# Kernel optimization log

Hardware: AMD Instinct MI355X
Metric: run time of the kernel (lower is better)

The kernel has to match this reference:

```python
import jax, jax.numpy as jnp
import numpy as np

D = 1024
H = 16
HD = D // H
SCALE = HD ** -0.5


def setup_inputs() -> dict:
    key = jax.random.key(0)
    ks = jax.random.split(key, 5)
    x = jax.random.normal(ks[0], (2, 2048, D), dtype=jnp.float32)
    s = 1.0 / np.sqrt(D)
    W_qkv = jax.random.uniform(ks[1], (D, 3 * D), jnp.float32, -s, s)
    b_qkv = jax.random.uniform(ks[2], (3 * D,), jnp.float32, -s, s)
    W_out = jax.random.uniform(ks[3], (D, D), jnp.float32, -s, s)
    b_out = jax.random.uniform(ks[4], (D,), jnp.float32, -s, s)
    return {"x": x, "W_qkv": W_qkv, "b_qkv": b_qkv, "W_out": W_out, "b_out": b_out}


def reference(x, W_qkv, b_qkv, W_out, b_out):
    B, S, _ = x.shape
    qkv = x @ W_qkv + b_qkv                       # [B,S,3D]
    qkv = qkv.reshape(B, S, 3, H, HD)
    q, k, v = jnp.moveaxis(qkv, 2, 0)             # each [B,S,H,HD]
    # scores: [B,H,S,S]
    scores = jnp.einsum("bshd,bthd->bhst", q, k) * SCALE
    attn = jax.nn.softmax(scores, axis=-1)        # dropout is identity in eval mode
    out = jnp.einsum("bhst,bthd->bshd", attn, v)  # [B,S,H,HD]
    out = out.reshape(B, S, H * HD)
    return out @ W_out + b_out
```

## Files before the change

### kernel.cpp

```cpp
#include <hip/hip_runtime.h>

typedef unsigned short u16;
typedef unsigned int   u32;

using short8 = __attribute__((ext_vector_type(8))) short;
using f32x4  = __attribute__((ext_vector_type(4))) float;
using half4  = __attribute__((ext_vector_type(4))) _Float16;
using half8  = __attribute__((ext_vector_type(8))) _Float16;

#define QSCALE 0.18033688011112042f

__device__ __forceinline__ u16 f2bf(float f) {
  u32 u = __float_as_uint(f);
  return (u16)((u + 0x8000u) >> 16);
}
__device__ __forceinline__ u16 f2h(float f) {
  _Float16 h = (_Float16)f;
  return __builtin_bit_cast(u16, h);
}

__device__ __forceinline__ void gld16(const u16* g, u16* l) {
  __builtin_amdgcn_global_load_lds(
      (const __attribute__((address_space(1))) unsigned int*)g,
      (__attribute__((address_space(3))) unsigned int*)l, 16, 0, 0);
}

__global__ __launch_bounds__(256) void cvt_x(const float* __restrict__ in,
                                             u16* __restrict__ out) {
  int idx = blockIdx.x * 256 + threadIdx.x;
  float4 v = reinterpret_cast<const float4*>(in)[idx];
  ushort4 o;
  o.x = f2bf(v.x); o.y = f2bf(v.y); o.z = f2bf(v.z); o.w = f2bf(v.w);
  reinterpret_cast<ushort4*>(out)[idx] = o;
}

__global__ __launch_bounds__(256) void transpose_w(const float* __restrict__ in,
                                                   u16* __restrict__ out,
                                                   int R, int C) {
  __shared__ u32 s[32][33];
  int c0 = blockIdx.x * 32, r0 = blockIdx.y * 32;
  int j = threadIdx.x & 31, i0 = threadIdx.x >> 5;
#pragma unroll
  for (int p = 0; p < 4; ++p) {
    int i = i0 + p * 8;
    s[i][j] = f2bf(in[(size_t)(r0 + i) * C + c0 + j]);
  }
  __syncthreads();
#pragma unroll
  for (int p = 0; p < 4; ++p) {
    int jj = i0 + p * 8;
    out[(size_t)(c0 + jj) * R + r0 + j] = (u16)s[j][jj];
  }
}

template <int EPI, int MT>
__global__ __launch_bounds__(256, 3) void gemm_bt(
    const u16* __restrict__ A, const u16* __restrict__ Bt,
    const float* __restrict__ bias, float* __restrict__ c_out,
    u16* __restrict__ q_out, u16* __restrict__ k_out, u16* __restrict__ vt_out,
    int M, int N, int K) {
  __shared__ __align__(16) u16 As[32 * MT * 32];
  __shared__ __align__(16) u16 Bs[128 * 32];
  const int tid = threadIdx.x;
  const int lane = tid & 63;
  const int wv = tid >> 6;
  const int l16 = lane & 15, quad = lane >> 4;
  const int wm = wv & 1, wn = wv >> 1;
  const int bx = blockIdx.x, by = blockIdx.y;

  const u16* Ab = A + (size_t)by * (32 * MT) * K;
  const u16* Bb = Bt + (size_t)bx * 128 * K;

  const f32x4 fzero = {0.0f, 0.0f, 0.0f, 0.0f};
  f32x4 acc[MT][4];
#pragma unroll
  for (int i = 0; i < MT; ++i)
#pragma unroll
    for (int j = 0; j < 4; ++j) acc[i][j] = fzero;

  for (int k0 = 0; k0 < K; k0 += 32) {
    __syncthreads();
#pragma unroll
    for (int p = 0; p < MT / 2; ++p) {
      int id = p * 256 + tid;
      int row = id >> 2, blk = id & 3;
      int gc = k0 + ((blk ^ (row & 3)) << 3);
      gld16(Ab + (size_t)row * K + gc, &As[id << 3]);
    }
#pragma unroll
    for (int p = 0; p < 2; ++p) {
      int id = p * 256 + tid;
      int row = id >> 2, blk = id & 3;
      int gc = k0 + ((blk ^ (row & 3)) << 3);
      gld16(Bb + (size_t)row * K + gc, &Bs[id << 3]);
    }
    __syncthreads();
    short8 af[MT], bfr[4];
#pragma unroll
    for (int mi = 0; mi < MT; ++mi) {
      int row = wm * (MT * 16) + mi * 16 + l16;
      af[mi] = *reinterpret_cast<const short8*>(&As[row * 32 + ((quad ^ (row & 3)) << 3)]);
    }
#pragma unroll
    for (int ni = 0; ni < 4; ++ni) {
      int row = wn * 64 + ni * 16 + l16;
      bfr[ni] = *reinterpret_cast<const short8*>(&Bs[row * 32 + ((quad ^ (row & 3)) << 3)]);
    }
#pragma unroll
    for (int mi = 0; mi < MT; ++mi)
#pragma unroll
      for (int ni = 0; ni < 4; ++ni)
        acc[mi][ni] = __builtin_amdgcn_mfma_f32_16x16x32_bf16(af[mi], bfr[ni], acc[mi][ni], 0, 0, 0);
  }

#pragma unroll
  for (int mi = 0; mi < MT; ++mi)
#pragma unroll
    for (int ni = 0; ni < 4; ++ni) {
      int col = bx * 128 + wn * 64 + ni * 16 + l16;
      float bv = bias[col];
      int row0 = by * (32 * MT) + wm * (MT * 16) + mi * 16 + quad * 4;
      if (EPI == 1) {
#pragma unroll
        for (int r = 0; r < 4; ++r)
          c_out[(size_t)(row0 + r) * N + col] = acc[mi][ni][r] + bv;
      } else {
        int which = col >> 10, rem = col & 1023;
        int h = rem >> 6, d = rem & 63;
        int b = row0 >> 11, sq0 = row0 & 2047;
        int bh = (b << 4) + h;
        if (which == 2) {
          ushort4 pk;
          pk.x = f2h(acc[mi][ni][0] + bv);
          pk.y = f2h(acc[mi][ni][1] + bv);
          pk.z = f2h(acc[mi][ni][2] + bv);
          pk.w = f2h(acc[mi][ni][3] + bv);
          size_t off = (size_t)bh * 131072 +
                       (((sq0 >> 2) * 16 + (d & 15)) * 16 + ((d >> 4) << 2));
          *reinterpret_cast<ushort4*>(&vt_out[off]) = pk;
        } else {
          size_t base = (size_t)(bh * 2048 + sq0) * 64 + d;
#pragma unroll
          for (int r = 0; r < 4; ++r) {
            float val = acc[mi][ni][r] + bv;
            if (which == 0) q_out[base + r * 64] = f2bf(val * QSCALE);
            else            k_out[base + r * 64] = f2bf(val);
          }
        }
      }
    }
}

__global__ __launch_bounds__(256, 4) void attn(
    const u16* __restrict__ q_buf, const u16* __restrict__ k_buf,
    const u16* __restrict__ vt_buf, u16* __restrict__ o_buf) {
  __shared__ __align__(16) u16 Ks[2][4096];
  __shared__ __align__(16) u16 Vs[2][4096];

  const int tid = threadIdx.x;
  const int lane = tid & 63, w = tid >> 6;
  const int l16 = lane & 15, quad = lane >> 4;
  const int bh = blockIdx.x, q0 = blockIdx.y * 64;

  const u16* qg = q_buf + (size_t)bh * 131072 + (q0 + w * 16) * 64;
  const u16* kg = k_buf + (size_t)bh * 131072;
  const u16* vg = vt_buf + (size_t)bh * 131072;

  short8 qb[2];
#pragma unroll
  for (int kk = 0; kk < 2; ++kk)
    qb[kk] = *reinterpret_cast<const short8*>(qg + l16 * 64 + kk * 32 + quad * 8);

  const int idA = tid, idB = 256 + tid;
  const u16* ksA = kg + (idA >> 3) * 64 + (((idA & 7) ^ ((idA >> 3) & 7)) << 3);
  const u16* ksB = kg + (idB >> 3) * 64 + (((idB & 7) ^ ((idB >> 3) & 7)) << 3);
  const u16* vsA = vg + ((idA ^ ((idA >> 4) & 1)) << 3);
  const u16* vsB = vg + ((idB ^ ((idB >> 4) & 1)) << 3);
  const int ldA = idA << 3, ldB = idB << 3;

  int k0o[4], k1o[4], v0o[4], v1o[4];
#pragma unroll
  for (int t = 0; t < 4; ++t) {
    int rr = t * 16 + l16;
    k0o[t] = rr * 64 + ((quad ^ (rr & 7)) << 3);
    k1o[t] = rr * 64 + (((4 + quad) ^ (rr & 7)) << 3);
    int gb = (t * 4 + quad) * 32 + l16 * 2;
    int sw = (l16 >> 3) & 1;
    v0o[t] = (gb + sw) << 3;
    v1o[t] = (gb + (sw ^ 1)) << 3;
  }

  const f32x4 fzero = {0.0f, 0.0f, 0.0f, 0.0f};
  f32x4 o_acc[4];
  float l_acc = 0.f;
#pragma unroll
  for (int nd = 0; nd < 4; ++nd) o_acc[nd] = fzero;

#define STAGE(BUF)                           \
  do {                                       \
    gld16(ksA, &Ks[BUF][ldA]);               \
    gld16(ksB, &Ks[BUF][ldB]);               \
    gld16(vsA, &Vs[BUF][ldA]);               \
    gld16(vsB, &Vs[BUF][ldB]);               \
    ksA += 4096; ksB += 4096;                \
    vsA += 4096; vsB += 4096;                \
  } while (0)

#define TILE(BUF)                                                         \
  do {                                                                    \
    _Pragma("unroll")                                                     \
    for (int t = 0; t < 4; ++t) {                                         \
      short8 k0f = *reinterpret_cast<const short8*>(&Ks[BUF][k0o[t]]);    \
      short8 k1f = *reinterpret_cast<const short8*>(&Ks[BUF][k1o[t]]);    \
      half8 v0 = *reinterpret_cast<const half8*>(&Vs[BUF][v0o[t]]);       \
      half8 v1 = *reinterpret_cast<const half8*>(&Vs[BUF][v1o[t]]);       \
      half4 vb0 = __builtin_shufflevector(v0, v0, 0, 1, 2, 3);            \
      half4 vb1 = __builtin_shufflevector(v0, v0, 4, 5, 6, 7);            \
      half4 vb2 = __builtin_shufflevector(v1, v1, 0, 1, 2, 3);            \
      half4 vb3 = __builtin_shufflevector(v1, v1, 4, 5, 6, 7);            \
      __builtin_amdgcn_s_setprio(1);                                      \
      f32x4 s = __builtin_amdgcn_mfma_f32_16x16x32_bf16(k0f, qb[0], fzero, 0, 0, 0); \
      s = __builtin_amdgcn_mfma_f32_16x16x32_bf16(k1f, qb[1], s, 0, 0, 0);\
      __builtin_amdgcn_s_setprio(0);                                      \
      float p0 = __builtin_amdgcn_exp2f(s[0]);                            \
      float p1 = __builtin_amdgcn_exp2f(s[1]);                            \
      float p2 = __builtin_amdgcn_exp2f(s[2]);                            \
      float p3 = __builtin_amdgcn_exp2f(s[3]);                            \
      l_acc += (p0 + p1) + (p2 + p3);                                     \
      half4 pa;                                                           \
      pa[0] = (_Float16)p0; pa[1] = (_Float16)p1;                         \
      pa[2] = (_Float16)p2; pa[3] = (_Float16)p3;                         \
      __builtin_amdgcn_s_setprio(1);                                      \
      o_acc[0] = __builtin_amdgcn_mfma_f32_16x16x16f16(pa, vb0, o_acc[0], 0, 0, 0); \
      o_acc[1] = __builtin_amdgcn_mfma_f32_16x16x16f16(pa, vb1, o_acc[1], 0, 0, 0); \
      o_acc[2] = __builtin_amdgcn_mfma_f32_16x16x16f16(pa, vb2, o_acc[2], 0, 0, 0); \
      o_acc[3] = __builtin_amdgcn_mfma_f32_16x16x16f16(pa, vb3, o_acc[3], 0, 0, 0); \
      __builtin_amdgcn_s_setprio(0);                                      \
    }                                                                     \
  } while (0)

  STAGE(0);
  __syncthreads();

  for (int i = 0; i < 32; i += 2) {
    if (i + 1 < 32) STAGE(1);
    TILE(0);
    __syncthreads();
    if (i + 2 < 32) STAGE(0);
    TILE(1);
    __syncthreads();
  }
#undef STAGE
#undef TILE

  l_acc += __shfl_xor(l_acc, 16, 64);
  l_acc += __shfl_xor(l_acc, 32, 64);

  const int b = bh >> 4, h = bh & 15;
  float lv[4];
#pragma unroll
  for (int r = 0; r < 4; ++r)
    lv[r] = __shfl(l_acc, quad * 4 + r, 64);
#pragma unroll
  for (int nd = 0; nd < 4; ++nd) {
#pragma unroll
    for (int r = 0; r < 4; ++r) {
      int sq = q0 + w * 16 + quad * 4 + r;
      o_buf[(size_t)(b * 2048 + sq) * 1024 + h * 64 + nd * 16 + l16] =
          f2bf(o_acc[nd][r] / lv[r]);
    }
  }
}

extern "C" void kernel_launch(void* const* d_in, const int* in_sizes, int n_in,
                              void* d_out, int out_size, void* d_ws, size_t ws_size,
                              hipStream_t stream) {
  (void)in_sizes; (void)n_in; (void)out_size; (void)ws_size;
  const float* x     = (const float*)d_in[0];
  const float* W_qkv = (const float*)d_in[1];
  const float* b_qkv = (const float*)d_in[2];
  const float* W_out = (const float*)d_in[3];
  const float* b_out = (const float*)d_in[4];
  float* out = (float*)d_out;

  char* ws = (char*)d_ws;
  u16* x_bf   = (u16*)(ws);
  u16* wqkv_t = (u16*)(ws + 8388608);
  u16* wout_t = (u16*)(ws + 14680064);
  u16* q_buf  = (u16*)(ws + 16777216);
  u16* k_buf  = (u16*)(ws + 25165824);
  u16* vt_buf = (u16*)(ws + 33554432);
  u16* o_bf   = (u16*)(ws + 41943040);

  cvt_x<<<4096, 256, 0, stream>>>(x, x_bf);
  transpose_w<<<dim3(96, 32), 256, 0, stream>>>(W_qkv, wqkv_t, 1024, 3072);
  transpose_w<<<dim3(32, 32), 256, 0, stream>>>(W_out, wout_t, 1024, 1024);
  gemm_bt<0, 4><<<dim3(24, 32), 256, 0, stream>>>(x_bf, wqkv_t, b_qkv, nullptr,
                                                  q_buf, k_buf, vt_buf, 4096, 3072, 1024);
  attn<<<dim3(32, 32), 256, 0, stream>>>(q_buf, k_buf, vt_buf, o_bf);
  gemm_bt<1, 2><<<dim3(8, 64), 256, 0, stream>>>(o_bf, wout_t, b_out, out,
                                                 nullptr, nullptr, nullptr, 4096, 1024, 1024);
}
```

Before: 189.0 us.

## Add dedicated QKV GEMM with 128x192 tiles and 4-stage LDS pipeline

Replaces the generic gemm_bt call for the QKV projection with a specialized kernel using 128x192 block tiles, a four-deep shared-memory ring buffer fed by direct global-to-LDS loads, and staged vmcnt waits. Loads for future tiles are interleaved between MFMA batches, with s_setprio raising priority around the matrix instructions, so memory latency overlaps compute. The larger tile raises register and LDS use, and occupancy drops to 2 blocks per SM. The grid shrinks to 512 blocks, which may load the 256 CUs unevenly.

```diff
diff --git a/kernel.cpp b/kernel.cpp
--- a/kernel.cpp
+++ b/kernel.cpp
@@ -51,6 +51,151 @@
     int jj = i0 + p * 8;
     out[(size_t)(c0 + jj) * R + r0 + j] = (u16)s[j][jj];
   }
+}
+
+__global__ __launch_bounds__(256, 2) void gemm_qkv(
+    const u16* __restrict__ A, const u16* __restrict__ Bt,
+    const float* __restrict__ bias,
+    u16* __restrict__ q_out, u16* __restrict__ k_out, u16* __restrict__ vt_out) {
+  const int K = 1024;
+  __shared__ __align__(16) u16 As[4][128 * 32];
+  __shared__ __align__(16) u16 Bs[4][192 * 32];
+  const int tid = threadIdx.x;
+  const int lane = tid & 63, wv = tid >> 6;
+  const int l16 = lane & 15, quad = lane >> 4;
+  const int wm = wv & 1, wn = wv >> 1;
+  const int bx = blockIdx.x, by = blockIdx.y;
+
+  const u16* Ab = A + (size_t)by * 128 * K;
+  const u16* Bb = Bt + (size_t)bx * 192 * K;
+
+  const int iA0 = tid, iA1 = 256 + tid;
+  const int iB0 = tid, iB1 = 256 + tid, iB2 = 512 + tid;
+  const u16* sA0 = Ab + (size_t)(iA0 >> 2) * K + (((iA0 & 3) ^ ((iA0 >> 2) & 3)) << 3);
+  const u16* sA1 = Ab + (size_t)(iA1 >> 2) * K + (((iA1 & 3) ^ ((iA1 >> 2) & 3)) << 3);
+  const u16* sB0 = Bb + (size_t)(iB0 >> 2) * K + (((iB0 & 3) ^ ((iB0 >> 2) & 3)) << 3);
+  const u16* sB1 = Bb + (size_t)(iB1 >> 2) * K + (((iB1 & 3) ^ ((iB1 >> 2) & 3)) << 3);
+  const u16* sB2 = Bb + (size_t)(iB2 >> 2) * K + (((iB2 & 3) ^ ((iB2 >> 2) & 3)) << 3);
+  const int dA0 = iA0 << 3, dA1 = iA1 << 3;
+  const int dB0 = iB0 << 3, dB1 = iB1 << 3, dB2 = iB2 << 3;
+
+  int aoff[4], boff[6];
+#pragma unroll
+  for (int mi = 0; mi < 4; ++mi) {
+    int r = wm * 64 + mi * 16 + l16;
+    aoff[mi] = r * 32 + ((quad ^ (r & 3)) << 3);
+  }
+#pragma unroll
+  for (int ni = 0; ni < 6; ++ni) {
+    int r = wn * 96 + ni * 16 + l16;
+    boff[ni] = r * 32 + ((quad ^ (r & 3)) << 3);
+  }
+
+  const f32x4 fzero = {0.0f, 0.0f, 0.0f, 0.0f};
+  f32x4 acc[4][6];
+#pragma unroll
+  for (int i = 0; i < 4; ++i)
+#pragma unroll
+    for (int j = 0; j < 6; ++j) acc[i][j] = fzero;
+
+#define STAGE_A(T)                        \
+  do {                                    \
+    gld16(sA0, &As[T][dA0]);              \
+    gld16(sA1, &As[T][dA1]);              \
+    sA0 += 32; sA1 += 32;                 \
+  } while (0)
+#define STAGE_B(T)                        \
+  do {                                    \
+    gld16(sB0, &Bs[T][dB0]);              \
+    gld16(sB1, &Bs[T][dB1]);              \
+    gld16(sB2, &Bs[T][dB2]);              \
+    sB0 += 32; sB1 += 32; sB2 += 32;      \
+  } while (0)
+#define VM5 asm volatile("s_waitcnt vmcnt(5)" ::: "memory")
+#define VM0 asm volatile("s_waitcnt vmcnt(0)" ::: "memory")
+
+#define GTILE(S, T, DOST, VW)                                              \
+  do {                                                                     \
+    short8 bb[6];                                                          \
+    _Pragma("unroll")                                                      \
+    for (int j = 0; j < 6; ++j)                                            \
+      bb[j] = *reinterpret_cast<const short8*>(&Bs[S][boff[j]]);           \
+    short8 a0 = *reinterpret_cast<const short8*>(&As[S][aoff[0]]);         \
+    short8 a1 = *reinterpret_cast<const short8*>(&As[S][aoff[1]]);         \
+    if (DOST) { STAGE_A(T); }                                              \
+    __builtin_amdgcn_s_barrier();                                          \
+    __builtin_amdgcn_s_setprio(1);                                         \
+    _Pragma("unroll")                                                      \
+    for (int j = 0; j < 6; ++j) {                                          \
+      acc[0][j] = __builtin_amdgcn_mfma_f32_16x16x32_bf16(a0, bb[j], acc[0][j], 0, 0, 0); \
+      acc[1][j] = __builtin_amdgcn_mfma_f32_16x16x32_bf16(a1, bb[j], acc[1][j], 0, 0, 0); \
+    }                                                                      \
+    __builtin_amdgcn_s_setprio(0);                                         \
+    __builtin_amdgcn_s_barrier();                                          \
+    short8 a2 = *reinterpret_cast<const short8*>(&As[S][aoff[2]]);         \
+    short8 a3 = *reinterpret_cast<const short8*>(&As[S][aoff[3]]);         \
+    if (DOST) { STAGE_B(T); }                                              \
+    __builtin_amdgcn_s_barrier();                                          \
+    __builtin_amdgcn_s_setprio(1);                                         \
+    _Pragma("unroll")                                                      \
+    for (int j = 0; j < 6; ++j) {                                          \
+      acc[2][j] = __builtin_amdgcn_mfma_f32_16x16x32_bf16(a2, bb[j], acc[2][j], 0, 0, 0); \
+      acc[3][j] = __builtin_amdgcn_mfma_f32_16x16x32_bf16(a3, bb[j], acc[3][j], 0, 0, 0); \
+    }                                                                      \
+    __builtin_amdgcn_s_setprio(0);                                         \
+    VW;                                                                    \
+    __builtin_amdgcn_s_barrier();                                          \
+  } while (0)
+
+  STAGE_A(0); STAGE_B(0);
+  STAGE_A(1); STAGE_B(1);
+  VM5;
+  __builtin_amdgcn_s_barrier();
+
+  for (int kb = 0; kb < 28; kb += 4) {
+    GTILE(0, 2, 1, VM5);
+    GTILE(1, 3, 1, VM5);
+    GTILE(2, 0, 1, VM5);
+    GTILE(3, 1, 1, VM5);
+  }
+  GTILE(0, 2, 1, VM5);
+  GTILE(1, 3, 1, VM5);
+  GTILE(2, 0, 0, VM0);
+  GTILE(3, 1, 0, ((void)0));
+#undef GTILE
+#undef STAGE_A
+#undef STAGE_B
+
+#pragma unroll
+  for (int mi = 0; mi < 4; ++mi)
+#pragma unroll
+    for (int ni = 0; ni < 6; ++ni) {
+      int col = bx * 192 + wn * 96 + ni * 16 + l16;
+      float bv = bias[col];
+      int row0 = by * 128 + wm * 64 + mi * 16 + quad * 4;
+      int which = col >> 10, rem = col & 1023;
+      int h = rem >> 6, d = rem & 63;
+      int b = row0 >> 11, sq0 = row0 & 2047;
+      int bh = (b << 4) + h;
+      if (which == 2) {
+        ushort4 pk;
+        pk.x = f2h(acc[mi][ni][0] + bv);
+        pk.y = f2h(acc[mi][ni][1] + bv);
+        pk.z = f2h(acc[mi][ni][2] + bv);
+        pk.w = f2h(acc[mi][ni][3] + bv);
+        size_t off = (size_t)bh * 131072 +
+                     (((sq0 >> 2) * 16 + (d & 15)) * 16 + ((d >> 4) << 2));
+        *reinterpret_cast<ushort4*>(&vt_out[off]) = pk;
+      } else {
+        size_t base = (size_t)(bh * 2048 + sq0) * 64 + d;
+#pragma unroll
+        for (int r = 0; r < 4; ++r) {
+          float val = acc[mi][ni][r] + bv;
+          if (which == 0) q_out[base + r * 64] = f2bf(val * QSCALE);
+          else            k_out[base + r * 64] = f2bf(val);
+        }
+      }
+    }
 }
 
 template <int EPI, int MT>
@@ -295,8 +440,8 @@
   cvt_x<<<4096, 256, 0, stream>>>(x, x_bf);
   transpose_w<<<dim3(96, 32), 256, 0, stream>>>(W_qkv, wqkv_t, 1024, 3072);
   transpose_w<<<dim3(32, 32), 256, 0, stream>>>(W_out, wout_t, 1024, 1024);
-  gemm_bt<0, 4><<<dim3(24, 32), 256, 0, stream>>>(x_bf, wqkv_t, b_qkv, nullptr,
-                                                  q_buf, k_buf, vt_buf, 4096, 3072, 1024);
+  gemm_qkv<<<dim3(16, 32), 256, 0, stream>>>(x_bf, wqkv_t, b_qkv,
+                                             q_buf, k_buf, vt_buf);
   attn<<<dim3(32, 32), 256, 0, stream>>>(q_buf, k_buf, vt_buf, o_bf);
   gemm_bt<1, 2><<<dim3(8, 64), 256, 0, stream>>>(o_bf, wout_t, b_out, out,
                                                  nullptr, nullptr, nullptr, 4096, 1024, 1024);
```

New measurement: 188.3 us. Within noise of the previous version (-0.3%).

## Double-buffer GEMM LDS tiles and retile to 64-row blocks with setprio

Applied to the files above, without the earlier changes.

Replaces the single-buffered GEMM with a double-buffered version that issues the next K-slice's global-to-LDS loads before computing the current one, so the loads overlap the MFMA work. Tiles change to 64 rows by NI*32 columns (192 columns for the QKV projection, 64 for the output projection), launch bounds rise to 4 blocks per SM, source pointers are precomputed, and s_setprio wraps the MFMA bursts. The aim is to hide global-load latency and keep more blocks resident. In exchange it doubles LDS per block, and the grids and per-wave register use change.

```diff
diff --git a/kernel.cpp b/kernel.cpp
--- a/kernel.cpp
+++ b/kernel.cpp
@@ -53,73 +53,105 @@
   }
 }
 
-template <int EPI, int MT>
-__global__ __launch_bounds__(256, 3) void gemm_bt(
+template <int EPI, int NI>
+__global__ __launch_bounds__(256, 4) void gemm4(
     const u16* __restrict__ A, const u16* __restrict__ Bt,
     const float* __restrict__ bias, float* __restrict__ c_out,
     u16* __restrict__ q_out, u16* __restrict__ k_out, u16* __restrict__ vt_out,
-    int M, int N, int K) {
-  __shared__ __align__(16) u16 As[32 * MT * 32];
-  __shared__ __align__(16) u16 Bs[128 * 32];
+    int N, int K) {
+  constexpr int BN = NI * 32;
+  constexpr int PB = BN / 64;
+  __shared__ __align__(16) u16 As[2][64 * 32];
+  __shared__ __align__(16) u16 Bs[2][BN * 32];
   const int tid = threadIdx.x;
-  const int lane = tid & 63;
-  const int wv = tid >> 6;
+  const int lane = tid & 63, wv = tid >> 6;
   const int l16 = lane & 15, quad = lane >> 4;
   const int wm = wv & 1, wn = wv >> 1;
   const int bx = blockIdx.x, by = blockIdx.y;
 
-  const u16* Ab = A + (size_t)by * (32 * MT) * K;
-  const u16* Bb = Bt + (size_t)bx * 128 * K;
+  const u16* Ab = A + (size_t)by * 64 * K;
+  const u16* Bb = Bt + (size_t)bx * BN * K;
+
+  const u16* sA = Ab + (size_t)(tid >> 2) * K + (((tid & 3) ^ ((tid >> 2) & 3)) << 3);
+  const int dA = tid << 3;
+  const u16* sB[PB];
+  int dB[PB];
+#pragma unroll
+  for (int p = 0; p < PB; ++p) {
+    int id = p * 256 + tid;
+    sB[p] = Bb + (size_t)(id >> 2) * K + (((id & 3) ^ ((id >> 2) & 3)) << 3);
+    dB[p] = id << 3;
+  }
+
+  int aoff[2], boff[NI];
+#pragma unroll
+  for (int mi = 0; mi < 2; ++mi) {
+    int r = wm * 32 + mi * 16 + l16;
+    aoff[mi] = r * 32 + ((quad ^ (r & 3)) << 3);
+  }
+#pragma unroll
+  for (int ni = 0; ni < NI; ++ni) {
+    int r = wn * (BN / 2) + ni * 16 + l16;
+    boff[ni] = r * 32 + ((quad ^ (r & 3)) << 3);
+  }
 
   const f32x4 fzero = {0.0f, 0.0f, 0.0f, 0.0f};
-  f32x4 acc[MT][4];
-#pragma unroll
-  for (int i = 0; i < MT; ++i)
-#pragma unroll
-    for (int j = 0; j < 4; ++j) acc[i][j] = fzero;
-
-  for (int k0 = 0; k0 < K; k0 += 32) {
+  f32x4 acc[2][NI];
+#pragma unroll
+  for (int i = 0; i < 2; ++i)
+#pragma unroll
+    for (int j = 0; j < NI; ++j) acc[i][j] = fzero;
+
+#define STAGE4(T)                                            \
+  do {                                                       \
+    gld16(sA, &As[T][dA]);                                   \
+    sA += 32;                                                \
+    _Pragma("unroll")                                        \
+    for (int p = 0; p < PB; ++p) {                           \
+      gld16(sB[p], &Bs[T][dB[p]]);                           \
+      sB[p] += 32;                                           \
+    }                                                        \
+  } while (0)
+
+#define KSTEP4(S)                                                          \
+  do {                                                                     \
+    short8 a0 = *reinterpret_cast<const short8*>(&As[S][aoff[0]]);         \
+    short8 a1 = *reinterpret_cast<const short8*>(&As[S][aoff[1]]);         \
+    short8 bb[NI];                                                         \
+    _Pragma("unroll")                                                      \
+    for (int j = 0; j < NI; ++j)                                           \
+      bb[j] = *reinterpret_cast<const short8*>(&Bs[S][boff[j]]);           \
+    __builtin_amdgcn_s_setprio(1);                                         \
+    _Pragma("unroll")                                                      \
+    for (int j = 0; j < NI; ++j) {                                         \
+      acc[0][j] = __builtin_amdgcn_mfma_f32_16x16x32_bf16(a0, bb[j], acc[0][j], 0, 0, 0); \
+      acc[1][j] = __builtin_amdgcn_mfma_f32_16x16x32_bf16(a1, bb[j], acc[1][j], 0, 0, 0); \
+    }                                                                      \
+    __builtin_amdgcn_s_setprio(0);                                         \
+  } while (0)
+
+  STAGE4(0);
+  __syncthreads();
+
+  const int NK = K / 32;
+  for (int ks = 0; ks < NK; ks += 2) {
+    if (ks + 1 < NK) STAGE4(1);
+    KSTEP4(0);
     __syncthreads();
-#pragma unroll
-    for (int p = 0; p < MT / 2; ++p) {
-      int id = p * 256 + tid;
-      int row = id >> 2, blk = id & 3;
-      int gc = k0 + ((blk ^ (row & 3)) << 3);
-      gld16(Ab + (size_t)row * K + gc, &As[id << 3]);
-    }
-#pragma unroll
-    for (int p = 0; p < 2; ++p) {
-      int id = p * 256 + tid;
-      int row = id >> 2, blk = id & 3;
-      int gc = k0 + ((blk ^ (row & 3)) << 3);
-      gld16(Bb + (size_t)row * K + gc, &Bs[id << 3]);
-    }
+    if (ks + 2 < NK) STAGE4(0);
+    KSTEP4(1);
     __syncthreads();
-    short8 af[MT], bfr[4];
-#pragma unroll
-    for (int mi = 0; mi < MT; ++mi) {
-      int row = wm * (MT * 16) + mi * 16 + l16;
-      af[mi] = *reinterpret_cast<const short8*>(&As[row * 32 + ((quad ^ (row & 3)) << 3)]);
-    }
-#pragma unroll
-    for (int ni = 0; ni < 4; ++ni) {
-      int row = wn * 64 + ni * 16 + l16;
-      bfr[ni] = *reinterpret_cast<const short8*>(&Bs[row * 32 + ((quad ^ (row & 3)) << 3)]);
-    }
-#pragma unroll
-    for (int mi = 0; mi < MT; ++mi)
-#pragma unroll
-      for (int ni = 0; ni < 4; ++ni)
-        acc[mi][ni] = __builtin_amdgcn_mfma_f32_16x16x32_bf16(af[mi], bfr[ni], acc[mi][ni], 0, 0, 0);
-  }
-
-#pragma unroll
-  for (int mi = 0; mi < MT; ++mi)
-#pragma unroll
-    for (int ni = 0; ni < 4; ++ni) {
-      int col = bx * 128 + wn * 64 + ni * 16 + l16;
+  }
+#undef STAGE4
+#undef KSTEP4
+
+#pragma unroll
+  for (int mi = 0; mi < 2; ++mi)
+#pragma unroll
+    for (int ni = 0; ni < NI; ++ni) {
+      int col = bx * BN + wn * (BN / 2) + ni * 16 + l16;
       float bv = bias[col];
-      int row0 = by * (32 * MT) + wm * (MT * 16) + mi * 16 + quad * 4;
+      int row0 = by * 64 + wm * 32 + mi * 16 + quad * 4;
       if (EPI == 1) {
 #pragma unroll
         for (int r = 0; r < 4; ++r)
@@ -295,9 +327,9 @@
   cvt_x<<<4096, 256, 0, stream>>>(x, x_bf);
   transpose_w<<<dim3(96, 32), 256, 0, stream>>>(W_qkv, wqkv_t, 1024, 3072);
   transpose_w<<<dim3(32, 32), 256, 0, stream>>>(W_out, wout_t, 1024, 1024);
-  gemm_bt<0, 4><<<dim3(24, 32), 256, 0, stream>>>(x_bf, wqkv_t, b_qkv, nullptr,
-                                                  q_buf, k_buf, vt_buf, 4096, 3072, 1024);
+  gemm4<0, 6><<<dim3(16, 64), 256, 0, stream>>>(x_bf, wqkv_t, b_qkv, nullptr,
+                                                q_buf, k_buf, vt_buf, 3072, 1024);
   attn<<<dim3(32, 32), 256, 0, stream>>>(q_buf, k_buf, vt_buf, o_bf);
-  gemm_bt<1, 2><<<dim3(8, 64), 256, 0, stream>>>(o_bf, wout_t, b_out, out,
-                                                 nullptr, nullptr, nullptr, 4096, 1024, 1024);
-}
+  gemm4<1, 2><<<dim3(16, 64), 256, 0, stream>>>(o_bf, wout_t, b_out, out,
+                                                nullptr, nullptr, nullptr, 1024, 1024);
+}
```

After: 195.6 us. 1.03x slower.
